# Performance work log

Measured on AMD Instinct MI355X. Metric: run time of the kernel, lower is better.

Reference implementation:

```python
import jax, jax.numpy as jnp
import numpy as np

# Model config (matches init_kwargs)
E, TOP_K, H, I = 16, 2, 2048, 1024
B, S = 2, 2048
GROUP = 16                 # NVFP4 quantization group size along contraction dim
RSF = 1.0                  # routed_scaling_factor


def setup_inputs() -> dict:
    key = jax.random.key(0)
    ks = jax.random.split(key, 6)
    hidden_states = jax.random.normal(ks[0], (B, S, H), dtype=jnp.float32)
    gate_weight = jax.random.normal(ks[1], (E, H), dtype=jnp.float32) * 0.02
    # int4 codes stored as int32 in [0,16); reference subtracts 8 -> [-8,7]
    fc_up_qweights = jax.random.randint(ks[2], (E, H, I), 0, 16, dtype=jnp.int32)
    fc_up_blocks_scale = jax.random.uniform(ks[3], (E, H // GROUP, I), dtype=jnp.float32) * 0.02
    fc_up_global_scale = jnp.ones((1,), dtype=jnp.float32)
    fc_down_qweights = jax.random.randint(ks[4], (E, I, H), 0, 16, dtype=jnp.int32)
    fc_down_blocks_scale = jax.random.uniform(ks[5], (E, I // GROUP, H), dtype=jnp.float32) * 0.02
    fc_down_global_scale = jnp.ones((1,), dtype=jnp.float32)
    return {
        'hidden_states': hidden_states,
        'gate_weight': gate_weight,
        'fc_up_blocks_scale': fc_up_blocks_scale,
        'fc_up_global_scale': fc_up_global_scale,
        'fc_down_blocks_scale': fc_down_blocks_scale,
        'fc_down_global_scale': fc_down_global_scale,
        'fc_up_qweights': fc_up_qweights,
        'fc_down_qweights': fc_down_qweights,
    }


def _dequant(q, blocks_scale, global_scale):
    # q: [E,K,N] int codes (0..15 -> -8..7); blocks_scale: [E,K/GROUP,N]
    e, k, n = q.shape
    w = (q.astype(jnp.float32) - 8.0).reshape(e, k // GROUP, GROUP, n)
    w = w * blocks_scale[:, :, None, :]
    return w.reshape(e, k, n) * global_scale[0]


def reference(hidden_states, gate_weight, fc_up_blocks_scale, fc_up_global_scale,
              fc_down_blocks_scale, fc_down_global_scale,
              fc_up_qweights, fc_down_qweights):
    b, s, h = hidden_states.shape
    x = hidden_states.reshape(-1, h).astype(jnp.float32)          # [T,H]
    t = x.shape[0]

    # Router: HF sigmoid routing mapped through logsigmoid so that
    # softmax(logsigmoid(l)) == sigmoid(l)/sum(sigmoid(l))  (nemotron_h_plugin_router_logits)
    logits = jax.nn.log_sigmoid(x @ gate_weight.T)                # [T,E]
    probs = jax.nn.softmax(logits, axis=-1)
    topw, topi = jax.lax.top_k(probs, TOP_K)                      # [T,K]
    topw = topw / (jnp.sum(topw, axis=-1, keepdims=True) + 1e-20) # renormalize

    # Dense per-token expert weights [T,E] (scatter of top-k weights)
    wdense = jnp.zeros((t, E), dtype=jnp.float32)
    wdense = wdense.at[jnp.arange(t)[:, None], topi].add(topw) * RSF

    w_up = _dequant(fc_up_qweights, fc_up_blocks_scale, fc_up_global_scale)     # [E,H,I]
    w_down = _dequant(fc_down_qweights, fc_down_blocks_scale, fc_down_global_scale)  # [E,I,H]

    z = jnp.einsum('th,ehi->tei', x, w_up)                        # up proj
    a = jnp.square(jnp.maximum(z, 0.0))                           # activation_type=0: ReLU^2
    aw = a * wdense[:, :, None]                                   # fold routing weights (linear)
    y = jnp.einsum('tei,eih->th', aw, w_down)                     # down proj + combine
    return y.reshape(b, s, h)
```

## Files before the change

kernel.cpp:

```cpp
#include <hip/hip_runtime.h>

#define TOK 4096
#define NE 16
#define HD 2048
#define ID 1024
#define QGROUP 16
#define CAP 4096

typedef _Float16 half4v __attribute__((ext_vector_type(4)));
typedef _Float16 half8v __attribute__((ext_vector_type(8)));
typedef float float4v __attribute__((ext_vector_type(4)));

__device__ __forceinline__ void g2l16(const void* g, void* l) {
    __builtin_amdgcn_global_load_lds(
        (const __attribute__((address_space(1))) unsigned int*)g,
        (__attribute__((address_space(3))) unsigned int*)l, 16, 0, 0);
}

__global__ __launch_bounds__(256) void prep_kernel(
    const float* __restrict__ x, _Float16* __restrict__ xh)
{
    int i8 = (blockIdx.x * 256 + threadIdx.x) * 8;
    float4 f0 = *(const float4*)&x[i8];
    float4 f1 = *(const float4*)&x[i8 + 4];
    half8v h;
    h[0] = (_Float16)f0.x; h[1] = (_Float16)f0.y; h[2] = (_Float16)f0.z; h[3] = (_Float16)f0.w;
    h[4] = (_Float16)f1.x; h[5] = (_Float16)f1.y; h[6] = (_Float16)f1.z; h[7] = (_Float16)f1.w;
    *(half8v*)&xh[i8] = h;
}

__global__ __launch_bounds__(256) void router_kernel(
    const float* __restrict__ x, const float* __restrict__ gw,
    int* __restrict__ topi, float* __restrict__ topw)
{
    int t = blockIdx.x;
    int tid = threadIdx.x;
    float p[NE];
#pragma unroll
    for (int e = 0; e < NE; e++) p[e] = 0.f;
    const float* xr = x + (size_t)t * HD;
    for (int h = tid; h < HD; h += 256) {
        float xv = xr[h];
#pragma unroll
        for (int e = 0; e < NE; e++) p[e] = fmaf(xv, gw[e * HD + h], p[e]);
    }
#pragma unroll
    for (int off = 32; off > 0; off >>= 1) {
#pragma unroll
        for (int e = 0; e < NE; e++) p[e] += __shfl_down(p[e], off, 64);
    }
    __shared__ float part[4][NE];
    int wave = tid >> 6, lane = tid & 63;
    if (lane == 0) {
#pragma unroll
        for (int e = 0; e < NE; e++) part[wave][e] = p[e];
    }
    __syncthreads();
    if (tid == 0) {
        float s[NE]; float sum = 0.f;
#pragma unroll
        for (int e = 0; e < NE; e++) {
            float l = part[0][e] + part[1][e] + part[2][e] + part[3][e];
            float sg = 1.f / (1.f + expf(-l));
            s[e] = sg; sum += sg;
        }
        int i1 = 0;
#pragma unroll
        for (int e = 1; e < NE; e++) if (s[e] > s[i1]) i1 = e;
        int i2 = (i1 == 0) ? 1 : 0;
#pragma unroll
        for (int e = 0; e < NE; e++) if (e != i1 && s[e] > s[i2]) i2 = e;
        float p1 = s[i1] / sum, p2 = s[i2] / sum;
        float inv = 1.f / (p1 + p2 + 1e-20f);
        topi[t * 2 + 0] = i1; topw[t * 2 + 0] = p1 * inv;
        topi[t * 2 + 1] = i2; topw[t * 2 + 1] = p2 * inv;
    }
}

__global__ __launch_bounds__(256) void compact_kernel(
    const int* __restrict__ topi, const float* __restrict__ topw,
    int* __restrict__ counts, int* __restrict__ pair_row, float* __restrict__ pair_w)
{
    const int e = blockIdx.x;
    const int tid = threadIdx.x;
    const int lane = tid & 63, wv = tid >> 6;
    __shared__ int wsum[4];
    int running = 0;
    for (int base = 0; base < 2 * TOK; base += 256) {
        const int idx = base + tid;
        const bool f = (topi[idx] == e);
        unsigned long long b = __ballot(f);
        int pre = __popcll(b & ((1ull << lane) - 1ull));
        if (lane == 0) wsum[wv] = __popcll(b);
        __syncthreads();
        int woff = 0;
#pragma unroll
        for (int w = 0; w < 4; w++) if (w < wv) woff += wsum[w];
        const int tot = wsum[0] + wsum[1] + wsum[2] + wsum[3];
        if (f) {
            const int pos = running + woff + pre;
            pair_row[e * CAP + pos] = idx;
            pair_w[e * CAP + pos] = topw[idx];
        }
        running += tot;
        __syncthreads();
    }
    if (tid == 0) counts[e] = running;
}

template<int K, int N>
__global__ __launch_bounds__(256) void dequantT_kernel(
    const int* __restrict__ qw, const float* __restrict__ bsc, _Float16* __restrict__ wq)
{
    const int e = blockIdx.z, kt = blockIdx.y, nt = blockIdx.x;
    const int tid = threadIdx.x;
    __shared__ _Float16 T[64][68];

    const int c4 = (tid & 15) * 4;
    const int r0 = tid >> 4;
#pragma unroll
    for (int p = 0; p < 4; p++) {
        const int r = p * 16 + r0;
        const int kabs = kt * 64 + r;
        const int4 c = *(const int4*)&qw[((size_t)e * K + kabs) * N + nt * 64 + c4];
        const float4 sc = *(const float4*)&bsc[((size_t)e * (K / QGROUP) + (kabs >> 4)) * N + nt * 64 + c4];
        half4v h;
        h[0] = (_Float16)((float)(c.x - 8) * sc.x);
        h[1] = (_Float16)((float)(c.y - 8) * sc.y);
        h[2] = (_Float16)((float)(c.z - 8) * sc.z);
        h[3] = (_Float16)((float)(c.w - 8) * sc.w);
        *(half4v*)&T[r][c4] = h;
    }
    __syncthreads();
    const int nrow = tid >> 2;
    const int kseg = (tid & 3) * 16;
    half8v o0, o1;
#pragma unroll
    for (int i = 0; i < 8; i++) o0[i] = T[kseg + i][nrow];
#pragma unroll
    for (int i = 0; i < 8; i++) o1[i] = T[kseg + 8 + i][nrow];
    _Float16* dst = wq + ((size_t)e * N + nt * 64 + nrow) * K + kt * 64 + kseg;
    *(half8v*)dst = o0;
    *(half8v*)(dst + 8) = o1;
}

template<int N, int K, bool UP>
__global__ __launch_bounds__(256) void gemm2_kernel(
    const _Float16* __restrict__ A, const _Float16* __restrict__ BT,
    const float* __restrict__ gsc,
    const int* __restrict__ counts, const int* __restrict__ pair_row,
    const float* __restrict__ pair_w,
    _Float16* __restrict__ store16, float* __restrict__ store32)
{
    constexpr int NT = N / 128;
    const int e = blockIdx.y;
    const int cnt = counts[e];
    const int mt = blockIdx.x / NT, nt = blockIdx.x % NT;
    const int mbase = mt * 128;
    if (mbase >= cnt) return;
    const int nbase = nt * 128;
    const int tid = threadIdx.x;

    __shared__ _Float16 As[128 * 32];
    __shared__ _Float16 Bs[128 * 32];
    __shared__ int rows_s[128];
    __shared__ float pw_s[128];

    if (tid < 128) {
        int idx = mbase + tid; if (idx >= cnt) idx = cnt - 1;
        rows_s[tid] = pair_row[e * CAP + idx];
        pw_s[tid] = UP ? pair_w[e * CAP + idx] : 0.f;
    }
    __syncthreads();

    const int lane = tid & 63, wv = tid >> 6;
    const int quad = lane >> 4, lm = lane & 15;
    const int wr = (wv >> 1) * 64, wc = (wv & 1) * 64;

    const int lsub = lane >> 2;
    const int lkof = (lane & 3) * 8;
    const _Float16* asrc[2];
    const _Float16* bsrc[2];
    _Float16* adst[2];
    _Float16* bdst[2];
#pragma unroll
    for (int i = 0; i < 2; i++) {
        const int lr = wv * 32 + i * 16 + lsub;
        const int pr = rows_s[lr];
        asrc[i] = A + (size_t)(UP ? (pr >> 1) : pr) * K + lkof;
        bsrc[i] = BT + ((size_t)e * N + nbase + lr) * K + lkof;
        adst[i] = &As[(wv * 32 + i * 16) * 32];
        bdst[i] = &Bs[(wv * 32 + i * 16) * 32];
    }

    float4v acc[4][4];
#pragma unroll
    for (int mi = 0; mi < 4; mi++)
#pragma unroll
        for (int ni = 0; ni < 4; ni++) acc[mi][ni] = (float4v){0.f, 0.f, 0.f, 0.f};

    for (int k0 = 0; k0 < K; k0 += 32) {
#pragma unroll
        for (int i = 0; i < 2; i++) {
            g2l16(asrc[i] + k0, adst[i]);
            g2l16(bsrc[i] + k0, bdst[i]);
        }
        __syncthreads();
        half8v af[4], bf[4];
#pragma unroll
        for (int mi = 0; mi < 4; mi++)
            af[mi] = *(const half8v*)&As[(wr + mi * 16 + lm) * 32 + quad * 8];
#pragma unroll
        for (int ni = 0; ni < 4; ni++)
            bf[ni] = *(const half8v*)&Bs[(wc + ni * 16 + lm) * 32 + quad * 8];
#pragma unroll
        for (int mi = 0; mi < 4; mi++)
#pragma unroll
            for (int ni = 0; ni < 4; ni++)
                acc[mi][ni] = __builtin_amdgcn_mfma_f32_16x16x32_f16(af[mi], bf[ni], acc[mi][ni], 0, 0, 0);
        __syncthreads();
    }

    const float gs = gsc[0];
#pragma unroll
    for (int mi = 0; mi < 4; mi++) {
#pragma unroll
        for (int r = 0; r < 4; r++) {
            const int rl = wr + mi * 16 + quad * 4 + r;
            if (mbase + rl < cnt) {
                const int pr = rows_s[rl];
#pragma unroll
                for (int ni = 0; ni < 4; ni++) {
                    const int col = nbase + wc + ni * 16 + lm;
                    float v = acc[mi][ni][r] * gs;
                    if (UP) {
                        v = fmaxf(v, 0.f);
                        v = v * v * pw_s[rl];
                        store16[(size_t)pr * N + col] = (_Float16)v;
                    } else {
                        atomicAdd(&store32[(size_t)(pr >> 1) * N + col], v);
                    }
                }
            }
        }
    }
}

template<int N, int K, bool UP>
__global__ __launch_bounds__(256) void gemm_fused_kernel(
    const _Float16* __restrict__ A, const int* __restrict__ qw,
    const float* __restrict__ bsc, const float* __restrict__ gsc,
    const int* __restrict__ counts, const int* __restrict__ pair_row,
    const float* __restrict__ pair_w,
    _Float16* __restrict__ store16, float* __restrict__ store32)
{
    constexpr int NT = N / 128;
    const int e = blockIdx.y;
    const int cnt = counts[e];
    const int mt = blockIdx.x / NT, nt = blockIdx.x % NT;
    const int mbase = mt * 128;
    if (mbase >= cnt) return;
    const int nbase = nt * 128;
    const int tid = threadIdx.x;

    __shared__ _Float16 As[128][40];
    __shared__ _Float16 Bs[128][40];
    __shared__ int rows_s[128];
    __shared__ float pw_s[128];

    if (tid < 128) {
        int idx = mbase + tid; if (idx >= cnt) idx = cnt - 1;
        rows_s[tid] = pair_row[e * CAP + idx];
        pw_s[tid] = UP ? pair_w[e * CAP + idx] : 0.f;
    }

    const int lane = tid & 63, wv = tid >> 6;
    const int quad = lane >> 4, lm = lane & 15;
    const int wr = (wv >> 1) * 64, wc = (wv & 1) * 64;

    float4v acc[4][4];
#pragma unroll
    for (int mi = 0; mi < 4; mi++)
#pragma unroll
        for (int ni = 0; ni < 4; ni++) acc[mi][ni] = (float4v){0.f, 0.f, 0.f, 0.f};

    const int am = tid & 127, akk = (tid >> 7) * 16;
    const int bn4 = (tid & 31) * 4, bkb = (tid >> 5) * 4;

    for (int k0 = 0; k0 < K; k0 += 32) {
        __syncthreads();
        {
            int pr = rows_s[am];
            const _Float16* src = A + (size_t)(UP ? (pr >> 1) : pr) * K + k0 + akk;
            *(uint4*)&As[am][akk] = *(const uint4*)src;
            *(uint4*)&As[am][akk + 8] = *(const uint4*)(src + 8);
        }
        {
            const int kabs = k0 + bkb;
            const float4 sc = *(const float4*)&bsc[((size_t)e * (K / QGROUP) + (kabs >> 4)) * N + nbase + bn4];
            const int4 c0 = *(const int4*)&qw[((size_t)e * K + kabs + 0) * N + nbase + bn4];
            const int4 c1 = *(const int4*)&qw[((size_t)e * K + kabs + 1) * N + nbase + bn4];
            const int4 c2 = *(const int4*)&qw[((size_t)e * K + kabs + 2) * N + nbase + bn4];
            const int4 c3 = *(const int4*)&qw[((size_t)e * K + kabs + 3) * N + nbase + bn4];
            half4v q;
            q[0] = (_Float16)((c0.x - 8) * sc.x); q[1] = (_Float16)((c1.x - 8) * sc.x);
            q[2] = (_Float16)((c2.x - 8) * sc.x); q[3] = (_Float16)((c3.x - 8) * sc.x);
            *(half4v*)&Bs[bn4 + 0][bkb] = q;
            q[0] = (_Float16)((c0.y - 8) * sc.y); q[1] = (_Float16)((c1.y - 8) * sc.y);
            q[2] = (_Float16)((c2.y - 8) * sc.y); q[3] = (_Float16)((c3.y - 8) * sc.y);
            *(half4v*)&Bs[bn4 + 1][bkb] = q;
            q[0] = (_Float16)((c0.z - 8) * sc.z); q[1] = (_Float16)((c1.z - 8) * sc.z);
            q[2] = (_Float16)((c2.z - 8) * sc.z); q[3] = (_Float16)((c3.z - 8) * sc.z);
            *(half4v*)&Bs[bn4 + 2][bkb] = q;
            q[0] = (_Float16)((c0.w - 8) * sc.w); q[1] = (_Float16)((c1.w - 8) * sc.w);
            q[2] = (_Float16)((c2.w - 8) * sc.w); q[3] = (_Float16)((c3.w - 8) * sc.w);
            *(half4v*)&Bs[bn4 + 3][bkb] = q;
        }
        __syncthreads();
        half8v af[4], bf[4];
#pragma unroll
        for (int mi = 0; mi < 4; mi++)
            af[mi] = *(const half8v*)&As[wr + mi * 16 + lm][quad * 8];
#pragma unroll
        for (int ni = 0; ni < 4; ni++)
            bf[ni] = *(const half8v*)&Bs[wc + ni * 16 + lm][quad * 8];
#pragma unroll
        for (int mi = 0; mi < 4; mi++)
#pragma unroll
            for (int ni = 0; ni < 4; ni++)
                acc[mi][ni] = __builtin_amdgcn_mfma_f32_16x16x32_f16(af[mi], bf[ni], acc[mi][ni], 0, 0, 0);
    }

    const float gs = gsc[0];
#pragma unroll
    for (int mi = 0; mi < 4; mi++) {
#pragma unroll
        for (int r = 0; r < 4; r++) {
            const int rl = wr + mi * 16 + quad * 4 + r;
            if (mbase + rl < cnt) {
                const int pr = rows_s[rl];
#pragma unroll
                for (int ni = 0; ni < 4; ni++) {
                    const int col = nbase + wc + ni * 16 + lm;
                    float v = acc[mi][ni][r] * gs;
                    if (UP) {
                        v = fmaxf(v, 0.f);
                        v = v * v * pw_s[rl];
                        store16[(size_t)pr * N + col] = (_Float16)v;
                    } else {
                        atomicAdd(&store32[(size_t)(pr >> 1) * N + col], v);
                    }
                }
            }
        }
    }
}

extern "C" void kernel_launch(void* const* d_in, const int* in_sizes, int n_in,
                              void* d_out, int out_size, void* d_ws, size_t ws_size,
                              hipStream_t stream) {
    const float* x   = (const float*)d_in[0];
    const float* gw  = (const float*)d_in[1];
    const float* usc = (const float*)d_in[2];
    const float* ugs = (const float*)d_in[3];
    const float* dsc = (const float*)d_in[4];
    const float* dgs = (const float*)d_in[5];
    const int*   uq  = (const int*)d_in[6];
    const int*   dq  = (const int*)d_in[7];
    float* out = (float*)d_out;

    char* ws = (char*)d_ws;
    int*   counts   = (int*)(ws + 0);
    int*   pair_row = (int*)(ws + 4096);
    float* pair_w   = (float*)(ws + 4096 + (size_t)NE * CAP * 4);
    _Float16* xh    = (_Float16*)(ws + 528384);
    _Float16* act   = (_Float16*)(ws + 528384 + (size_t)TOK * HD * 2);
    _Float16* wq    = (_Float16*)(ws + 528384 + (size_t)TOK * HD * 2
                                  + (size_t)2 * TOK * ID * 2);
    int*   topi = (int*)wq;
    float* topw = (float*)((char*)wq + (size_t)2 * TOK * 4);
    const size_t need_deq = 34082816ull + (size_t)NE * HD * ID * 2;
    const bool use_deq = ws_size >= need_deq;

    hipMemsetAsync(out, 0, (size_t)TOK * HD * 4, stream);

    prep_kernel<<<(TOK * HD) / (256 * 8), 256, 0, stream>>>(x, xh);
    router_kernel<<<TOK, 256, 0, stream>>>(x, gw, topi, topw);
    compact_kernel<<<NE, 256, 0, stream>>>(topi, topw, counts, pair_row, pair_w);

    if (use_deq) {
        dequantT_kernel<HD, ID><<<dim3(ID / 64, HD / 64, NE), 256, 0, stream>>>(uq, usc, wq);
        gemm2_kernel<ID, HD, true><<<dim3((CAP / 128) * (ID / 128), NE), 256, 0, stream>>>(
            xh, wq, ugs, counts, pair_row, pair_w, act, nullptr);
        dequantT_kernel<ID, HD><<<dim3(HD / 64, ID / 64, NE), 256, 0, stream>>>(dq, dsc, wq);
        gemm2_kernel<HD, ID, false><<<dim3((CAP / 128) * (HD / 128), NE), 256, 0, stream>>>(
            act, wq, dgs, counts, pair_row, pair_w, nullptr, out);
    } else {
        gemm_fused_kernel<ID, HD, true><<<dim3((CAP / 128) * (ID / 128), NE), 256, 0, stream>>>(
            xh, uq, usc, ugs, counts, pair_row, pair_w, act, nullptr);
        gemm_fused_kernel<HD, ID, false><<<dim3((CAP / 128) * (HD / 128), NE), 256, 0, stream>>>(
            act, dq, dsc, dgs, counts, pair_row, pair_w, nullptr, out);
    }
}
```

Before: 541.2 us.

## Warp-specialize grouped GEMM with producer waves and double-buffered swizzled LDS

Replaces the single-buffer grouped MoE GEMM with a 512-thread variant. Four producer waves issue global-to-LDS loads into a double-buffered, XOR-swizzled 64-wide K tile while four consumer waves run MFMAs on the other buffer. This aims to hide global load latency, cut LDS bank conflicts and halve the number of barriers per K. The cost is twice the LDS footprint and idle producer waves holding register and occupancy budget. The pipelining also relies on the async g2l loads being complete at each barrier, which depends on implicit vmcnt waits before s_barrier.

```diff
diff --git a/kernel.cpp b/kernel.cpp
--- a/kernel.cpp
+++ b/kernel.cpp
@@ -145,7 +145,7 @@
 }
 
 template<int N, int K, bool UP>
-__global__ __launch_bounds__(256) void gemm2_kernel(
+__global__ __launch_bounds__(512, 4) void gemm3_kernel(
     const _Float16* __restrict__ A, const _Float16* __restrict__ BT,
     const float* __restrict__ gsc,
     const int* __restrict__ counts, const int* __restrict__ pair_row,
@@ -153,6 +153,7 @@
     _Float16* __restrict__ store16, float* __restrict__ store32)
 {
     constexpr int NT = N / 128;
+    constexpr int ITERS = K / 64;
     const int e = blockIdx.y;
     const int cnt = counts[e];
     const int mt = blockIdx.x / NT, nt = blockIdx.x % NT;
@@ -161,8 +162,8 @@
     const int nbase = nt * 128;
     const int tid = threadIdx.x;
 
-    __shared__ _Float16 As[128 * 32];
-    __shared__ _Float16 Bs[128 * 32];
+    __shared__ _Float16 As[2][128 * 64];
+    __shared__ _Float16 Bs[2][128 * 64];
     __shared__ int rows_s[128];
     __shared__ float pw_s[128];
 
@@ -173,53 +174,77 @@
     }
     __syncthreads();
 
-    const int lane = tid & 63, wv = tid >> 6;
+    const int wv = tid >> 6, lane = tid & 63;
+    const bool producer = (wv >= 4);
+
+    const _Float16* aptr[4];
+    const _Float16* bptr[4];
+    int pw = 0;
+    if (producer) {
+        pw = wv - 4;
+        const int rsub = lane >> 3;
+        const int gch = (lane & 7) ^ rsub;
+#pragma unroll
+        for (int j = 0; j < 4; j++) {
+            const int r = pw * 32 + j * 8 + rsub;
+            const int pr = rows_s[r];
+            aptr[j] = A + (size_t)(UP ? (pr >> 1) : pr) * K + gch * 8;
+            bptr[j] = BT + ((size_t)e * N + nbase + r) * K + gch * 8;
+        }
+        _Float16* ab = &As[0][pw * 32 * 64];
+        _Float16* bb = &Bs[0][pw * 32 * 64];
+#pragma unroll
+        for (int j = 0; j < 4; j++) {
+            g2l16(aptr[j], ab + j * 512);
+            g2l16(bptr[j], bb + j * 512);
+        }
+    }
+
     const int quad = lane >> 4, lm = lane & 15;
     const int wr = (wv >> 1) * 64, wc = (wv & 1) * 64;
 
-    const int lsub = lane >> 2;
-    const int lkof = (lane & 3) * 8;
-    const _Float16* asrc[2];
-    const _Float16* bsrc[2];
-    _Float16* adst[2];
-    _Float16* bdst[2];
-#pragma unroll
-    for (int i = 0; i < 2; i++) {
-        const int lr = wv * 32 + i * 16 + lsub;
-        const int pr = rows_s[lr];
-        asrc[i] = A + (size_t)(UP ? (pr >> 1) : pr) * K + lkof;
-        bsrc[i] = BT + ((size_t)e * N + nbase + lr) * K + lkof;
-        adst[i] = &As[(wv * 32 + i * 16) * 32];
-        bdst[i] = &Bs[(wv * 32 + i * 16) * 32];
-    }
-
     float4v acc[4][4];
 #pragma unroll
     for (int mi = 0; mi < 4; mi++)
 #pragma unroll
         for (int ni = 0; ni < 4; ni++) acc[mi][ni] = (float4v){0.f, 0.f, 0.f, 0.f};
 
-    for (int k0 = 0; k0 < K; k0 += 32) {
-#pragma unroll
-        for (int i = 0; i < 2; i++) {
-            g2l16(asrc[i] + k0, adst[i]);
-            g2l16(bsrc[i] + k0, bdst[i]);
-        }
+    for (int it = 0; it < ITERS; it++) {
         __syncthreads();
-        half8v af[4], bf[4];
-#pragma unroll
-        for (int mi = 0; mi < 4; mi++)
-            af[mi] = *(const half8v*)&As[(wr + mi * 16 + lm) * 32 + quad * 8];
-#pragma unroll
-        for (int ni = 0; ni < 4; ni++)
-            bf[ni] = *(const half8v*)&Bs[(wc + ni * 16 + lm) * 32 + quad * 8];
-#pragma unroll
-        for (int mi = 0; mi < 4; mi++)
-#pragma unroll
-            for (int ni = 0; ni < 4; ni++)
-                acc[mi][ni] = __builtin_amdgcn_mfma_f32_16x16x32_f16(af[mi], bf[ni], acc[mi][ni], 0, 0, 0);
-        __syncthreads();
-    }
+        if (producer) {
+            if (it + 1 < ITERS) {
+                const int nb = (it + 1) & 1;
+                const int kof = (it + 1) * 64;
+                _Float16* ab = &As[nb][pw * 32 * 64];
+                _Float16* bb = &Bs[nb][pw * 32 * 64];
+#pragma unroll
+                for (int j = 0; j < 4; j++) {
+                    g2l16(aptr[j] + kof, ab + j * 512);
+                    g2l16(bptr[j] + kof, bb + j * 512);
+                }
+            }
+        } else {
+            const int buf = it & 1;
+#pragma unroll
+            for (int ks = 0; ks < 2; ks++) {
+                const int s = ((ks * 4 + quad) ^ (lm & 7)) * 8;
+                half8v af[4], bf[4];
+#pragma unroll
+                for (int mi = 0; mi < 4; mi++)
+                    af[mi] = *(const half8v*)&As[buf][(wr + mi * 16 + lm) * 64 + s];
+#pragma unroll
+                for (int ni = 0; ni < 4; ni++)
+                    bf[ni] = *(const half8v*)&Bs[buf][(wc + ni * 16 + lm) * 64 + s];
+#pragma unroll
+                for (int mi = 0; mi < 4; mi++)
+#pragma unroll
+                    for (int ni = 0; ni < 4; ni++)
+                        acc[mi][ni] = __builtin_amdgcn_mfma_f32_16x16x32_f16(af[mi], bf[ni], acc[mi][ni], 0, 0, 0);
+            }
+        }
+    }
+
+    if (producer) return;
 
     const float gs = gsc[0];
 #pragma unroll
@@ -390,10 +415,10 @@
 
     if (use_deq) {
         dequantT_kernel<HD, ID><<<dim3(ID / 64, HD / 64, NE), 256, 0, stream>>>(uq, usc, wq);
-        gemm2_kernel<ID, HD, true><<<dim3((CAP / 128) * (ID / 128), NE), 256, 0, stream>>>(
+        gemm3_kernel<ID, HD, true><<<dim3((CAP / 128) * (ID / 128), NE), 512, 0, stream>>>(
             xh, wq, ugs, counts, pair_row, pair_w, act, nullptr);
         dequantT_kernel<ID, HD><<<dim3(HD / 64, ID / 64, NE), 256, 0, stream>>>(dq, dsc, wq);
-        gemm2_kernel<HD, ID, false><<<dim3((CAP / 128) * (HD / 128), NE), 256, 0, stream>>>(
+        gemm3_kernel<HD, ID, false><<<dim3((CAP / 128) * (HD / 128), NE), 512, 0, stream>>>(
             act, wq, dgs, counts, pair_row, pair_w, nullptr, out);
     } else {
         gemm_fused_kernel<ID, HD, true><<<dim3((CAP / 128) * (ID / 128), NE), 256, 0, stream>>>(
```

Result: no change. 549.3 us (+1.5%).

## Shrink grouped GEMM M-tile to 64 with grouped block swizzle and occupancy hint

Applied to the files above, without the earlier changes.

Replaces the 128x128 expert GEMM tile with a 64x128 tile, so each wave computes a 32x64 sub-block with fewer accumulators. Blocks launch on a flattened 1D grid with an 8-wide swizzle so that neighbouring blocks share the same expert/N-tile weights, and launch_bounds now requests 4 blocks per CU. The aim is less padding waste when per-expert token counts are uneven, better L2 reuse of the weight tiles, and higher occupancy. In exchange, B tiles are reloaded from global memory twice as often and each block does less MFMA work per LDS load.

```diff
diff --git a/kernel.cpp b/kernel.cpp
--- a/kernel.cpp
+++ b/kernel.cpp
@@ -145,7 +145,7 @@
 }
 
 template<int N, int K, bool UP>
-__global__ __launch_bounds__(256) void gemm2_kernel(
+__global__ __launch_bounds__(256, 4) void gemm4_kernel(
     const _Float16* __restrict__ A, const _Float16* __restrict__ BT,
     const float* __restrict__ gsc,
     const int* __restrict__ counts, const int* __restrict__ pair_row,
@@ -153,68 +153,64 @@
     _Float16* __restrict__ store16, float* __restrict__ store32)
 {
     constexpr int NT = N / 128;
-    const int e = blockIdx.y;
+    constexpr int MT = CAP / 64;
+    const int bx = blockIdx.x;
+    const int g8 = bx & 7;
+    const int rest = bx >> 3;
+    const int m = rest % MT;
+    const int g = (rest / MT) * 8 + g8;
+    const int e = g / NT, nt = g % NT;
     const int cnt = counts[e];
-    const int mt = blockIdx.x / NT, nt = blockIdx.x % NT;
-    const int mbase = mt * 128;
+    const int mbase = m * 64;
     if (mbase >= cnt) return;
     const int nbase = nt * 128;
     const int tid = threadIdx.x;
 
-    __shared__ _Float16 As[128 * 32];
+    __shared__ _Float16 As[64 * 32];
     __shared__ _Float16 Bs[128 * 32];
-    __shared__ int rows_s[128];
-    __shared__ float pw_s[128];
-
-    if (tid < 128) {
+    __shared__ int rows_s[64];
+    __shared__ float pw_s[64];
+
+    if (tid < 64) {
         int idx = mbase + tid; if (idx >= cnt) idx = cnt - 1;
         rows_s[tid] = pair_row[e * CAP + idx];
         pw_s[tid] = UP ? pair_w[e * CAP + idx] : 0.f;
     }
     __syncthreads();
 
+    const int arow = tid >> 2, akc = tid & 3;
+    const int pra = rows_s[arow];
+    const _Float16* asrc  = A + (size_t)(UP ? (pra >> 1) : pra) * K + akc * 8;
+    const _Float16* bsrc0 = BT + ((size_t)e * N + nbase + arow) * K + akc * 8;
+    const _Float16* bsrc1 = bsrc0 + (size_t)64 * K;
+    _Float16* adst  = &As[tid * 8];
+    _Float16* bdst0 = &Bs[tid * 8];
+    _Float16* bdst1 = &Bs[2048 + tid * 8];
+
     const int lane = tid & 63, wv = tid >> 6;
     const int quad = lane >> 4, lm = lane & 15;
-    const int wr = (wv >> 1) * 64, wc = (wv & 1) * 64;
-
-    const int lsub = lane >> 2;
-    const int lkof = (lane & 3) * 8;
-    const _Float16* asrc[2];
-    const _Float16* bsrc[2];
-    _Float16* adst[2];
-    _Float16* bdst[2];
-#pragma unroll
-    for (int i = 0; i < 2; i++) {
-        const int lr = wv * 32 + i * 16 + lsub;
-        const int pr = rows_s[lr];
-        asrc[i] = A + (size_t)(UP ? (pr >> 1) : pr) * K + lkof;
-        bsrc[i] = BT + ((size_t)e * N + nbase + lr) * K + lkof;
-        adst[i] = &As[(wv * 32 + i * 16) * 32];
-        bdst[i] = &Bs[(wv * 32 + i * 16) * 32];
-    }
-
-    float4v acc[4][4];
-#pragma unroll
-    for (int mi = 0; mi < 4; mi++)
+    const int wm = (wv & 1) * 32, wn = (wv >> 1) * 64;
+
+    float4v acc[2][4];
+#pragma unroll
+    for (int mi = 0; mi < 2; mi++)
 #pragma unroll
         for (int ni = 0; ni < 4; ni++) acc[mi][ni] = (float4v){0.f, 0.f, 0.f, 0.f};
 
     for (int k0 = 0; k0 < K; k0 += 32) {
-#pragma unroll
-        for (int i = 0; i < 2; i++) {
-            g2l16(asrc[i] + k0, adst[i]);
-            g2l16(bsrc[i] + k0, bdst[i]);
-        }
-        __syncthreads();
-        half8v af[4], bf[4];
-#pragma unroll
-        for (int mi = 0; mi < 4; mi++)
-            af[mi] = *(const half8v*)&As[(wr + mi * 16 + lm) * 32 + quad * 8];
+        g2l16(asrc + k0, adst);
+        g2l16(bsrc0 + k0, bdst0);
+        g2l16(bsrc1 + k0, bdst1);
+        __syncthreads();
+        half8v af[2], bf[4];
+#pragma unroll
+        for (int mi = 0; mi < 2; mi++)
+            af[mi] = *(const half8v*)&As[(wm + mi * 16 + lm) * 32 + quad * 8];
 #pragma unroll
         for (int ni = 0; ni < 4; ni++)
-            bf[ni] = *(const half8v*)&Bs[(wc + ni * 16 + lm) * 32 + quad * 8];
-#pragma unroll
-        for (int mi = 0; mi < 4; mi++)
+            bf[ni] = *(const half8v*)&Bs[(wn + ni * 16 + lm) * 32 + quad * 8];
+#pragma unroll
+        for (int mi = 0; mi < 2; mi++)
 #pragma unroll
             for (int ni = 0; ni < 4; ni++)
                 acc[mi][ni] = __builtin_amdgcn_mfma_f32_16x16x32_f16(af[mi], bf[ni], acc[mi][ni], 0, 0, 0);
@@ -223,15 +219,15 @@
 
     const float gs = gsc[0];
 #pragma unroll
-    for (int mi = 0; mi < 4; mi++) {
+    for (int mi = 0; mi < 2; mi++) {
 #pragma unroll
         for (int r = 0; r < 4; r++) {
-            const int rl = wr + mi * 16 + quad * 4 + r;
+            const int rl = wm + mi * 16 + quad * 4 + r;
             if (mbase + rl < cnt) {
                 const int pr = rows_s[rl];
 #pragma unroll
                 for (int ni = 0; ni < 4; ni++) {
-                    const int col = nbase + wc + ni * 16 + lm;
+                    const int col = nbase + wn + ni * 16 + lm;
                     float v = acc[mi][ni][r] * gs;
                     if (UP) {
                         v = fmaxf(v, 0.f);
@@ -390,10 +386,10 @@
 
     if (use_deq) {
         dequantT_kernel<HD, ID><<<dim3(ID / 64, HD / 64, NE), 256, 0, stream>>>(uq, usc, wq);
-        gemm2_kernel<ID, HD, true><<<dim3((CAP / 128) * (ID / 128), NE), 256, 0, stream>>>(
+        gemm4_kernel<ID, HD, true><<<(CAP / 64) * (ID / 128) * NE, 256, 0, stream>>>(
             xh, wq, ugs, counts, pair_row, pair_w, act, nullptr);
         dequantT_kernel<ID, HD><<<dim3(HD / 64, ID / 64, NE), 256, 0, stream>>>(dq, dsc, wq);
-        gemm2_kernel<HD, ID, false><<<dim3((CAP / 128) * (HD / 128), NE), 256, 0, stream>>>(
+        gemm4_kernel<HD, ID, false><<<(CAP / 64) * (HD / 128) * NE, 256, 0, stream>>>(
             act, wq, dgs, counts, pair_row, pair_w, nullptr, out);
     } else {
         gemm_fused_kernel<ID, HD, true><<<dim3((CAP / 128) * (ID / 128), NE), 256, 0, stream>>>(
```

Measured after the change: 582.0 us. +7.5%, slower.
